# Kernel optimization log

Hardware: AMD Instinct MI355X
Metric: run time of the kernel (lower is better)

The kernel has to match this reference:

```python
import jax, jax.numpy as jnp
import numpy as np

H, I, B = 256, 128, 512

def setup_inputs() -> dict:
    key = jax.random.key(0)
    ks = jax.random.split(key, 24)
    n = lambda k, shp, s=1.0: jax.random.normal(k, shp, dtype=jnp.float32) * s
    inp = {
        "x": n(ks[0], (B, I)),
        "hx": n(ks[1], (B, H), 0.1),
        "cx": n(ks[2], (B, H, H), 0.1),
        # input->gate weights (hidden, input), xavier-like scale
        "Wii": n(ks[3], (H, I), (2.0 / (H + I)) ** 0.5),
        "Wif": n(ks[4], (H, I), (2.0 / (H + I)) ** 0.5),
        "Wig": n(ks[5], (H, I), (2.0 / (H + I)) ** 0.5),
        "Wio": n(ks[6], (H, I), (2.0 / (H + I)) ** 0.5),
        # hidden->gate weights (hidden, hidden), ~orthogonal scale
        "Whi": n(ks[7], (H, H), H ** -0.5),
        "Whit": n(ks[8], (H, H), H ** -0.5),
        "Whf": n(ks[9], (H, H), H ** -0.5),
        "Whft": n(ks[10], (H, H), H ** -0.5),
        "Whc": n(ks[11], (H, H), H ** -0.5),
        "Whct": n(ks[12], (H, H), H ** -0.5),
        "Who": n(ks[13], (H, H), H ** -0.5),
        "Uinv": n(ks[14], (H, H), H ** -0.5),
        "Vtinv": n(ks[15], (H, H), H ** -0.5),
        # biases: bi/bf/bg are full (H,H) matrices, bo is (H,1)
        "bi": jnp.zeros((H, H), jnp.float32),
        "bf": jnp.zeros((H, H), jnp.float32),
        "bg": jnp.zeros((H, H), jnp.float32),
        "bo": jnp.zeros((H, 1), jnp.float32),
    }
    return inp


def reference(x, hx, cx, Wii, Wif, Wig, Wio, Whi, Whit, Whf, Whft, Whc, Whct, Who, Uinv, Vtinv, bi, bf, bg, bo):
    # W @ diag(v) @ M^T  ==  einsum('hi,bi,gi->bhg', W, v, M)
    def sandwich(Wx, Wh, Wht, b):
        # (Wx*x) @ Wx^T + (Wh*hx) @ Wht^T + b  -> (B,H,H)
        xt = jnp.einsum('hi,bi,gi->bhg', Wx, x, Wx)
        ht = jnp.einsum('hj,bj,gj->bhg', Wh, hx, Wht)
        return xt + ht + b

    i = jax.nn.sigmoid(sandwich(Wii, Whi, Whit, bi))
    f = jax.nn.sigmoid(sandwich(Wif, Whf, Whft, bf))
    g = jnp.tanh(sandwich(Wig, Whc, Whct, bg))
    # o: ordinary vector gate (B,H)
    o = jax.nn.sigmoid(jnp.einsum('hi,bi->bh', Wio, x)
                       + jnp.einsum('hj,bj->bh', Who, hx) + bo[:, 0])
    cx_new = f * cx + i * g                     # (B,H,H)
    # diag(Uinv @ cx_new @ Vtinv) per batch element -> (B,H)
    proj_down = jnp.einsum('ij,bjk,ki->bi', Uinv, cx_new, Vtinv)
    hx_new = o * jax.nn.sigmoid(proj_down)
    return hx_new
```

## Files before the change

kernel.cpp:

```cpp
#include <hip/hip_runtime.h>
#include <hip/hip_bf16.h>

#define Hh 256
#define Ii 128
#define KF 384
#define LDSB 72

typedef __attribute__((ext_vector_type(8))) short bf16x8;
typedef __attribute__((ext_vector_type(4))) float f32x4;
typedef unsigned short u16;
typedef unsigned int u32;

__device__ inline u16 f2bf(float f) {
  u32 u = __float_as_uint(f);
  u += 0x7FFFu + ((u >> 16) & 1u);
  return (u16)(u >> 16);
}
__device__ inline u32 pack_bf16x2(float a, float b) {
  __hip_bfloat162 h = __float22bfloat162_rn(make_float2(a, b));
  u32 r; __builtin_memcpy(&r, &h, 4); return r;
}
__device__ inline u32 scale2(u32 packed, float va, float vb) {
  float lo = __uint_as_float(packed << 16) * va;
  float hi = __uint_as_float(packed & 0xFFFF0000u) * vb;
  return pack_bf16x2(lo, hi);
}
__device__ inline float sigm(float x) { return 1.0f / (1.0f + __expf(-x)); }
__device__ inline float tanh_f(float x) { return 1.0f - 2.0f / (1.0f + __expf(2.0f * x)); }

union U32x4 { bf16x8 f; u32 d[4]; uint4 v; };

__global__ __launch_bounds__(256) void k_prep(
    const float* __restrict__ Wii, const float* __restrict__ Wif, const float* __restrict__ Wig,
    const float* __restrict__ Whi, const float* __restrict__ Whit,
    const float* __restrict__ Whf, const float* __restrict__ Whft,
    const float* __restrict__ Whc, const float* __restrict__ Whct,
    const float* __restrict__ Vtinv, const float* __restrict__ Uinv,
    u16* __restrict__ RW, u16* __restrict__ CW, u16* __restrict__ Vtt,
    float* __restrict__ UinvP, float* __restrict__ proj) {
  const int tid = threadIdx.x, bx = blockIdx.x, y = blockIdx.y;
  if (y < 3) {
    const float* WX  = (y == 0) ? Wii : (y == 1 ? Wif : Wig);
    const float* WHr = (y == 0) ? Whi : (y == 1 ? Whf : Whc);
    const float* WHt = (y == 0) ? Whit : (y == 1 ? Whft : Whct);
    u16* rw = RW + y * Hh * KF;
    u16* cw = CW + y * Hh * KF;
#pragma unroll
    for (int it = 0; it < 4; ++it) {
      int idx = it * 24576 + bx * 256 + tid;
      int h = idx / KF, t = idx - h * KF;
      float a, c;
      if (t < Ii) { a = WX[h * Ii + t]; c = a; }
      else        { a = WHr[h * Hh + t - Ii]; c = WHt[h * Hh + t - Ii]; }
      rw[idx] = f2bf(a);
      cw[idx] = f2bf(c);
    }
  } else if (y == 3) {
    if (bx < 64) {
      __shared__ u16 tbuf[32][33];
      const int c = tid & 31, r8 = tid >> 5;
      const int tr = bx >> 3, tc = bx & 7;
#pragma unroll
      for (int rr = r8; rr < 32; rr += 8)
        tbuf[rr][c] = f2bf(Vtinv[(tc * 32 + rr) * Hh + tr * 32 + c]);
      __syncthreads();
#pragma unroll
      for (int rr = r8; rr < 32; rr += 8)
        Vtt[(tr * 32 + rr) * Hh + tc * 32 + c] = tbuf[c][rr];
    } else if (bx < 96) {
      const int base = (bx - 64) * 256 + tid;
      const float4 z = {0.f, 0.f, 0.f, 0.f};
#pragma unroll
      for (int it = 0; it < 4; ++it)
        *(float4*)(proj + (size_t)(it * 8192 + base) * 4) = z;
    }
  } else {
    if (bx < 32) {
      const int base = (bx * 256 + tid) * 8;
#pragma unroll
      for (int e8 = 0; e8 < 8; ++e8) {
        int f = base + e8;
        int t512 = f >> 7;
        int e = f & 127;
        int ti = e >> 5;
        int rem = e & 31;
        int tjl = rem >> 2;
        int rr = rem & 3;
        int wv = t512 >> 6;
        int ln = t512 & 63;
        int qd = ln >> 4;
        int r15v = ln & 15;
        int i = (wv & 3) * 64 + ti * 16 + qd * 4 + rr;
        int j = (wv >> 2) * 128 + tjl * 16 + r15v;
        UinvP[f] = Uinv[i * Hh + j];
      }
    }
  }
}

__global__ __launch_bounds__(512) void k_main(
    const float* __restrict__ x, const float* __restrict__ hx, const float* __restrict__ cx,
    const u16* __restrict__ RW, const u16* __restrict__ CW, const u16* __restrict__ Vtt,
    const float* __restrict__ bi, const float* __restrict__ bfm, const float* __restrict__ bg,
    const float* __restrict__ UinvP, float* __restrict__ proj) {
  __shared__ u16 sB[2 * 64 * LDSB];
  __shared__ u16 sP[256 * LDSB];
  __shared__ float sV[KF];
  __shared__ float sPart[8][64];

  const int tid  = threadIdx.x;
  const int b    = blockIdx.x >> 2;
  const int kb   = blockIdx.x & 3;
  const int k0   = kb * 64;
  const int lane = tid & 63;
  const int w    = tid >> 6;
  const int r15  = lane & 15;
  const int quad = lane >> 4;
  const int brow = tid >> 3, bcg = tid & 7;

  if (tid < Ii) sV[tid] = x[b * Ii + tid];
  if (tid < Hh) sV[Ii + tid] = hx[b * Hh + tid];

  const u16* rwp[3] = {RW + 2 * Hh * KF, RW, RW + 1 * Hh * KF};
  const u16* cwp[3] = {CW + 2 * Hh * KF, CW, CW + 1 * Hh * KF};
  const float* bp3[3] = {bg, bi, bfm};
  const float* cx_b = cx + (size_t)b * Hh * Hh;

  U32x4 m;
  m.v = *(const uint4*)(cwp[0] + (size_t)(k0 + brow) * KF + bcg * 8);
  __syncthreads();
  {
    U32x4 o;
    const float4 va = *(const float4*)(&sV[bcg * 8]);
    const float4 vb = *(const float4*)(&sV[bcg * 8 + 4]);
    o.d[0] = scale2(m.d[0], va.x, va.y); o.d[1] = scale2(m.d[1], va.z, va.w);
    o.d[2] = scale2(m.d[2], vb.x, vb.y); o.d[3] = scale2(m.d[3], vb.z, vb.w);
    *(uint4*)(&sB[brow * LDSB + bcg * 8]) = o.v;
  }
  __syncthreads();

  float p[2][4][4];
  const size_t wrow = (size_t)(w * 32 + r15) * KF;

#pragma unroll
  for (int ph = 0; ph < 3; ++ph) {
    f32x4 acc[2][4];
#pragma unroll
    for (int ja = 0; ja < 2; ++ja)
#pragma unroll
      for (int tk = 0; tk < 4; ++tk)
#pragma unroll
        for (int r = 0; r < 4; ++r) acc[ja][tk][r] = 0.0f;

#pragma unroll
    for (int kc = 0; kc < 6; ++kc) {
      const int sc  = ph * 6 + kc;
      const int cur = sc & 1;
      const int t0  = kc * 64;
      const int nph = (kc < 5) ? ph : (ph < 2 ? ph + 1 : 0);
      const int nt0 = (kc < 5) ? t0 + 64 : 0;
      U32x4 mn;
      if (sc < 17)
        mn.v = *(const uint4*)(cwp[nph] + (size_t)(k0 + brow) * KF + nt0 + bcg * 8);
      bf16x8 wf[2][2];
#pragma unroll
      for (int ja = 0; ja < 2; ++ja)
#pragma unroll
        for (int ks = 0; ks < 2; ++ks)
          wf[ja][ks] = *(const bf16x8*)(rwp[ph] + wrow + (size_t)ja * 16 * KF + t0 + ks * 32 + quad * 8);
#pragma unroll
      for (int ks = 0; ks < 2; ++ks) {
        bf16x8 sf[4];
#pragma unroll
        for (int tk = 0; tk < 4; ++tk)
          sf[tk] = *(const bf16x8*)(&sB[cur * (64 * LDSB) + (tk * 16 + r15) * LDSB + ks * 32 + quad * 8]);
#pragma unroll
        for (int tk = 0; tk < 4; ++tk) {
          acc[0][tk] = __builtin_amdgcn_mfma_f32_16x16x32_bf16(sf[tk], wf[0][ks], acc[0][tk], 0, 0, 0);
          acc[1][tk] = __builtin_amdgcn_mfma_f32_16x16x32_bf16(sf[tk], wf[1][ks], acc[1][tk], 0, 0, 0);
        }
      }
      if (sc < 17) {
        U32x4 o;
        const float4 va = *(const float4*)(&sV[nt0 + bcg * 8]);
        const float4 vb = *(const float4*)(&sV[nt0 + bcg * 8 + 4]);
        o.d[0] = scale2(mn.d[0], va.x, va.y); o.d[1] = scale2(mn.d[1], va.z, va.w);
        o.d[2] = scale2(mn.d[2], vb.x, vb.y); o.d[3] = scale2(mn.d[3], vb.z, vb.w);
        *(uint4*)(&sB[(cur ^ 1) * (64 * LDSB) + brow * LDSB + bcg * 8]) = o.v;
      }
      if (kc == 5) {
        const float* bp = bp3[ph];
#pragma unroll
        for (int ja = 0; ja < 2; ++ja) {
          const int jg = w * 32 + ja * 16 + r15;
          const float* bpr = bp + (size_t)jg * Hh + k0 + quad * 4;
          const float* cxr = cx_b + (size_t)jg * Hh + k0 + quad * 4;
#pragma unroll
          for (int tk = 0; tk < 4; ++tk) {
            const float4 bv = *(const float4*)(bpr + tk * 16);
            if (ph == 0) {
#pragma unroll
              for (int r = 0; r < 4; ++r)
                p[ja][tk][r] = tanh_f(acc[ja][tk][r] + ((const float*)&bv)[r]);
            } else if (ph == 1) {
#pragma unroll
              for (int r = 0; r < 4; ++r)
                p[ja][tk][r] *= sigm(acc[ja][tk][r] + ((const float*)&bv)[r]);
            } else {
              const float4 cv = *(const float4*)(cxr + tk * 16);
              float cc[4];
#pragma unroll
              for (int r = 0; r < 4; ++r)
                cc[r] = sigm(acc[ja][tk][r] + ((const float*)&bv)[r]) * ((const float*)&cv)[r] + p[ja][tk][r];
              uint2 pk;
              pk.x = pack_bf16x2(cc[0], cc[1]);
              pk.y = pack_bf16x2(cc[2], cc[3]);
              *(uint2*)(&sP[jg * LDSB + tk * 16 + quad * 4]) = pk;
            }
          }
        }
      }
      __syncthreads();
    }
  }

  const int islab = (w & 3) * 64;
  const int jhb   = (w >> 2) * 128;
  const float* up = UinvP + (size_t)tid * 128;
  float racc[4][4];
#pragma unroll
  for (int ti = 0; ti < 4; ++ti)
#pragma unroll
    for (int r = 0; r < 4; ++r) racc[ti][r] = 0.0f;

#pragma unroll
  for (int tjg = 0; tjg < 2; ++tjg) {
    bf16x8 fbp[2][4];
#pragma unroll
    for (int ks = 0; ks < 2; ++ks)
#pragma unroll
      for (int tjj = 0; tjj < 4; ++tjj)
        fbp[ks][tjj] = *(const bf16x8*)(&sP[(jhb + (tjg * 4 + tjj) * 16 + r15) * LDSB + ks * 32 + quad * 8]);
#pragma unroll
    for (int ti = 0; ti < 4; ++ti) {
      const u16* vrow = Vtt + (size_t)(islab + ti * 16 + r15) * Hh + k0 + quad * 8;
      const bf16x8 va0 = *(const bf16x8*)vrow;
      const bf16x8 va1 = *(const bf16x8*)(vrow + 32);
      f32x4 pacc[4];
#pragma unroll
      for (int tjj = 0; tjj < 4; ++tjj)
#pragma unroll
        for (int r = 0; r < 4; ++r) pacc[tjj][r] = 0.0f;
#pragma unroll
      for (int tjj = 0; tjj < 4; ++tjj)
        pacc[tjj] = __builtin_amdgcn_mfma_f32_16x16x32_bf16(va0, fbp[0][tjj], pacc[tjj], 0, 0, 0);
#pragma unroll
      for (int tjj = 0; tjj < 4; ++tjj)
        pacc[tjj] = __builtin_amdgcn_mfma_f32_16x16x32_bf16(va1, fbp[1][tjj], pacc[tjj], 0, 0, 0);
#pragma unroll
      for (int tjj = 0; tjj < 4; ++tjj) {
        const float4 uu = *(const float4*)(up + ti * 32 + (tjg * 4 + tjj) * 4);
#pragma unroll
        for (int r = 0; r < 4; ++r)
          racc[ti][r] += pacc[tjj][r] * ((const float*)&uu)[r];
      }
    }
  }

#pragma unroll
  for (int ti = 0; ti < 4; ++ti)
#pragma unroll
    for (int r = 0; r < 4; ++r) {
      float v = racc[ti][r];
      v += __shfl_xor(v, 1);
      v += __shfl_xor(v, 2);
      v += __shfl_xor(v, 4);
      v += __shfl_xor(v, 8);
      if (r15 == 0) sPart[w][ti * 16 + quad * 4 + r] = v;
    }
  __syncthreads();
  if (tid < Hh)
    atomicAdd(&proj[b * Hh + tid], sPart[tid >> 6][tid & 63] + sPart[(tid >> 6) + 4][tid & 63]);
}

__global__ __launch_bounds__(256) void k_out(
    const float* __restrict__ x, const float* __restrict__ hx,
    const float* __restrict__ Wio, const float* __restrict__ Who,
    const float* __restrict__ bo, const float* __restrict__ proj,
    float* __restrict__ out) {
  __shared__ float sv[KF];
  const int b = blockIdx.x, tid = threadIdx.x;
  const int lane = tid & 63, w = tid >> 6;
  if (tid < Ii) sv[tid] = x[b * Ii + tid];
  sv[Ii + tid] = hx[b * Hh + tid];
  __syncthreads();
  for (int rr = 0; rr < 64; ++rr) {
    const int h = w * 64 + rr;
    float p = Wio[h * Ii + lane]        * sv[lane]
            + Wio[h * Ii + 64 + lane]   * sv[64 + lane]
            + Who[h * Hh + lane]        * sv[128 + lane]
            + Who[h * Hh + 64 + lane]   * sv[192 + lane]
            + Who[h * Hh + 128 + lane]  * sv[256 + lane]
            + Who[h * Hh + 192 + lane]  * sv[320 + lane];
    p += __shfl_xor(p, 32);
    p += __shfl_xor(p, 16);
    p += __shfl_xor(p, 8);
    p += __shfl_xor(p, 4);
    p += __shfl_xor(p, 2);
    p += __shfl_xor(p, 1);
    if (lane == 0)
      out[b * Hh + h] = sigm(p + bo[h]) * sigm(proj[b * Hh + h]);
  }
}

extern "C" void kernel_launch(void* const* d_in, const int* in_sizes, int n_in,
                              void* d_out, int out_size, void* d_ws, size_t ws_size,
                              hipStream_t stream) {
  (void)in_sizes; (void)n_in; (void)out_size; (void)ws_size;
  const float* x    = (const float*)d_in[0];
  const float* hx   = (const float*)d_in[1];
  const float* cx   = (const float*)d_in[2];
  const float* Wii  = (const float*)d_in[3];
  const float* Wif  = (const float*)d_in[4];
  const float* Wig  = (const float*)d_in[5];
  const float* Wio  = (const float*)d_in[6];
  const float* Whi  = (const float*)d_in[7];
  const float* Whit = (const float*)d_in[8];
  const float* Whf  = (const float*)d_in[9];
  const float* Whft = (const float*)d_in[10];
  const float* Whc  = (const float*)d_in[11];
  const float* Whct = (const float*)d_in[12];
  const float* Who  = (const float*)d_in[13];
  const float* Uinv = (const float*)d_in[14];
  const float* Vtinv= (const float*)d_in[15];
  const float* bi   = (const float*)d_in[16];
  const float* bf   = (const float*)d_in[17];
  const float* bg   = (const float*)d_in[18];
  const float* bo   = (const float*)d_in[19];
  float* out = (float*)d_out;

  u16* RW    = (u16*)d_ws;
  u16* CW    = RW + 3 * Hh * KF;
  u16* Vtt   = CW + 3 * Hh * KF;
  float* UinvP = (float*)(Vtt + Hh * Hh);
  float* proj  = UinvP + Hh * Hh;

  k_prep<<<dim3(96, 5), 256, 0, stream>>>(Wii, Wif, Wig, Whi, Whit, Whf, Whft, Whc, Whct,
                                          Vtinv, Uinv, RW, CW, Vtt, UinvP, proj);
  k_main<<<2048, 512, 0, stream>>>(x, hx, cx, RW, CW, Vtt, bi, bf, bg, UinvP, proj);
  k_out<<<512, 256, 0, stream>>>(x, hx, Wio, Who, bo, proj, out);
}
```

Baseline: 583.4 us.

## Retile gate GEMM with wider K chunks and 4x2 warp tiles, union LDS buffers

The gate-stage GEMM now uses K chunks of 192 instead of 64, so each phase takes 2 steps instead of 6, cutting the number of __syncthreads and double-buffer refills. Warps are rearranged into a 4x2 (j by k) grid with 4x2 MFMA tiles, so each B fragment loaded from LDS is reused across four weight fragments. The B staging buffer and the P buffer share one LDS union, and the final f-gate/cell update moves after the loop with an extra barrier. In exchange, register pressure rises (more global loads per step, larger staging buffers), and the padded stride of 200 may cause LDS bank conflicts.

Result: slower. 708.9 us (+21.5%).

```diff
diff --git a/kernel.cpp b/kernel.cpp
--- a/kernel.cpp
+++ b/kernel.cpp
@@ -5,6 +5,8 @@
 #define Ii 128
 #define KF 384
 #define LDSB 72
+#define BK 192
+#define SBST 200
 
 typedef __attribute__((ext_vector_type(8))) short bf16x8;
 typedef __attribute__((ext_vector_type(4))) float f32x4;
@@ -27,8 +29,6 @@
 }
 __device__ inline float sigm(float x) { return 1.0f / (1.0f + __expf(-x)); }
 __device__ inline float tanh_f(float x) { return 1.0f - 2.0f / (1.0f + __expf(2.0f * x)); }
-
-union U32x4 { bf16x8 f; u32 d[4]; uint4 v; };
 
 __global__ __launch_bounds__(256) void k_prep(
     const float* __restrict__ Wii, const float* __restrict__ Wif, const float* __restrict__ Wig,
@@ -103,8 +103,10 @@
     const u16* __restrict__ RW, const u16* __restrict__ CW, const u16* __restrict__ Vtt,
     const float* __restrict__ bi, const float* __restrict__ bfm, const float* __restrict__ bg,
     const float* __restrict__ UinvP, float* __restrict__ proj) {
-  __shared__ u16 sB[2 * 64 * LDSB];
-  __shared__ u16 sP[256 * LDSB];
+  __shared__ union {
+    u16 B[2][64][SBST];
+    u16 P[256][LDSB];
+  } sU;
   __shared__ float sV[KF];
   __shared__ float sPart[8][64];
 
@@ -114,9 +116,12 @@
   const int k0   = kb * 64;
   const int lane = tid & 63;
   const int w    = tid >> 6;
+  const int wj   = w >> 1;
+  const int wk   = w & 1;
   const int r15  = lane & 15;
   const int quad = lane >> 4;
-  const int brow = tid >> 3, bcg = tid & 7;
+  const int srow = tid >> 3;
+  const int scg  = tid & 7;
 
   if (tid < Ii) sV[tid] = x[b * Ii + tid];
   if (tid < Hh) sV[Ii + tid] = hx[b * Hh + tid];
@@ -126,96 +131,122 @@
   const float* bp3[3] = {bg, bi, bfm};
   const float* cx_b = cx + (size_t)b * Hh * Hh;
 
-  U32x4 m;
-  m.v = *(const uint4*)(cwp[0] + (size_t)(k0 + brow) * KF + bcg * 8);
+  uint4 m0, m1, m2;
+  {
+    const u16* src = cwp[0] + (size_t)(k0 + srow) * KF + scg * 24;
+    m0 = *(const uint4*)src;
+    m1 = *(const uint4*)(src + 8);
+    m2 = *(const uint4*)(src + 16);
+  }
   __syncthreads();
   {
-    U32x4 o;
-    const float4 va = *(const float4*)(&sV[bcg * 8]);
-    const float4 vb = *(const float4*)(&sV[bcg * 8 + 4]);
-    o.d[0] = scale2(m.d[0], va.x, va.y); o.d[1] = scale2(m.d[1], va.z, va.w);
-    o.d[2] = scale2(m.d[2], vb.x, vb.y); o.d[3] = scale2(m.d[3], vb.z, vb.w);
-    *(uint4*)(&sB[brow * LDSB + bcg * 8]) = o.v;
+    const float* vp = &sV[scg * 24];
+    const float4 v0 = *(const float4*)(vp);
+    const float4 v1 = *(const float4*)(vp + 4);
+    const float4 v2 = *(const float4*)(vp + 8);
+    const float4 v3 = *(const float4*)(vp + 12);
+    const float4 v4 = *(const float4*)(vp + 16);
+    const float4 v5 = *(const float4*)(vp + 20);
+    uint4 o0, o1, o2;
+    o0.x = scale2(m0.x, v0.x, v0.y); o0.y = scale2(m0.y, v0.z, v0.w);
+    o0.z = scale2(m0.z, v1.x, v1.y); o0.w = scale2(m0.w, v1.z, v1.w);
+    o1.x = scale2(m1.x, v2.x, v2.y); o1.y = scale2(m1.y, v2.z, v2.w);
+    o1.z = scale2(m1.z, v3.x, v3.y); o1.w = scale2(m1.w, v3.z, v3.w);
+    o2.x = scale2(m2.x, v4.x, v4.y); o2.y = scale2(m2.y, v4.z, v4.w);
+    o2.z = scale2(m2.z, v5.x, v5.y); o2.w = scale2(m2.w, v5.z, v5.w);
+    u16* dst = &sU.B[0][srow][scg * 24];
+    *(uint4*)dst = o0;
+    *(uint4*)(dst + 8) = o1;
+    *(uint4*)(dst + 16) = o2;
   }
   __syncthreads();
 
-  float p[2][4][4];
-  const size_t wrow = (size_t)(w * 32 + r15) * KF;
+  float p[4][2][4];
+  f32x4 acc[4][2];
+  const size_t jrow = (size_t)(wj * 64 + r15) * KF;
+  const int ar = wk * 32 + r15;
 
 #pragma unroll
   for (int ph = 0; ph < 3; ++ph) {
-    f32x4 acc[2][4];
-#pragma unroll
-    for (int ja = 0; ja < 2; ++ja)
-#pragma unroll
-      for (int tk = 0; tk < 4; ++tk)
+#pragma unroll
+    for (int ja = 0; ja < 4; ++ja)
+#pragma unroll
+      for (int tk = 0; tk < 2; ++tk)
 #pragma unroll
         for (int r = 0; r < 4; ++r) acc[ja][tk][r] = 0.0f;
 
 #pragma unroll
-    for (int kc = 0; kc < 6; ++kc) {
-      const int sc  = ph * 6 + kc;
+    for (int kc = 0; kc < 2; ++kc) {
+      const int sc  = ph * 2 + kc;
       const int cur = sc & 1;
-      const int t0  = kc * 64;
-      const int nph = (kc < 5) ? ph : (ph < 2 ? ph + 1 : 0);
-      const int nt0 = (kc < 5) ? t0 + 64 : 0;
-      U32x4 mn;
-      if (sc < 17)
-        mn.v = *(const uint4*)(cwp[nph] + (size_t)(k0 + brow) * KF + nt0 + bcg * 8);
-      bf16x8 wf[2][2];
-#pragma unroll
-      for (int ja = 0; ja < 2; ++ja)
-#pragma unroll
-        for (int ks = 0; ks < 2; ++ks)
-          wf[ja][ks] = *(const bf16x8*)(rwp[ph] + wrow + (size_t)ja * 16 * KF + t0 + ks * 32 + quad * 8);
-#pragma unroll
-      for (int ks = 0; ks < 2; ++ks) {
-        bf16x8 sf[4];
-#pragma unroll
-        for (int tk = 0; tk < 4; ++tk)
-          sf[tk] = *(const bf16x8*)(&sB[cur * (64 * LDSB) + (tk * 16 + r15) * LDSB + ks * 32 + quad * 8]);
-#pragma unroll
-        for (int tk = 0; tk < 4; ++tk) {
-          acc[0][tk] = __builtin_amdgcn_mfma_f32_16x16x32_bf16(sf[tk], wf[0][ks], acc[0][tk], 0, 0, 0);
-          acc[1][tk] = __builtin_amdgcn_mfma_f32_16x16x32_bf16(sf[tk], wf[1][ks], acc[1][tk], 0, 0, 0);
-        }
-      }
-      if (sc < 17) {
-        U32x4 o;
-        const float4 va = *(const float4*)(&sV[nt0 + bcg * 8]);
-        const float4 vb = *(const float4*)(&sV[nt0 + bcg * 8 + 4]);
-        o.d[0] = scale2(mn.d[0], va.x, va.y); o.d[1] = scale2(mn.d[1], va.z, va.w);
-        o.d[2] = scale2(mn.d[2], vb.x, vb.y); o.d[3] = scale2(mn.d[3], vb.z, vb.w);
-        *(uint4*)(&sB[(cur ^ 1) * (64 * LDSB) + brow * LDSB + bcg * 8]) = o.v;
-      }
-      if (kc == 5) {
+      const int t0  = kc * BK;
+      uint4 n0, n1, n2;
+      if (sc < 5) {
+        const int nsc = sc + 1;
+        const int nph = nsc >> 1;
+        const int nt0 = (nsc & 1) * BK;
+        const u16* src = cwp[nph] + (size_t)(k0 + srow) * KF + nt0 + scg * 24;
+        n0 = *(const uint4*)src;
+        n1 = *(const uint4*)(src + 8);
+        n2 = *(const uint4*)(src + 16);
+      }
+      const u16* rb = rwp[ph] + jrow + t0 + quad * 8;
+#pragma unroll
+      for (int ksl = 0; ksl < 6; ++ksl) {
+        const bf16x8 sf0 = *(const bf16x8*)(&sU.B[cur][ar][ksl * 32 + quad * 8]);
+        const bf16x8 sf1 = *(const bf16x8*)(&sU.B[cur][ar + 16][ksl * 32 + quad * 8]);
+        const bf16x8 wf0 = *(const bf16x8*)(rb + ksl * 32);
+        const bf16x8 wf1 = *(const bf16x8*)(rb + 16 * KF + ksl * 32);
+        const bf16x8 wf2 = *(const bf16x8*)(rb + 32 * KF + ksl * 32);
+        const bf16x8 wf3 = *(const bf16x8*)(rb + 48 * KF + ksl * 32);
+        acc[0][0] = __builtin_amdgcn_mfma_f32_16x16x32_bf16(sf0, wf0, acc[0][0], 0, 0, 0);
+        acc[0][1] = __builtin_amdgcn_mfma_f32_16x16x32_bf16(sf1, wf0, acc[0][1], 0, 0, 0);
+        acc[1][0] = __builtin_amdgcn_mfma_f32_16x16x32_bf16(sf0, wf1, acc[1][0], 0, 0, 0);
+        acc[1][1] = __builtin_amdgcn_mfma_f32_16x16x32_bf16(sf1, wf1, acc[1][1], 0, 0, 0);
+        acc[2][0] = __builtin_amdgcn_mfma_f32_16x16x32_bf16(sf0, wf2, acc[2][0], 0, 0, 0);
+        acc[2][1] = __builtin_amdgcn_mfma_f32_16x16x32_bf16(sf1, wf2, acc[2][1], 0, 0, 0);
+        acc[3][0] = __builtin_amdgcn_mfma_f32_16x16x32_bf16(sf0, wf3, acc[3][0], 0, 0, 0);
+        acc[3][1] = __builtin_amdgcn_mfma_f32_16x16x32_bf16(sf1, wf3, acc[3][1], 0, 0, 0);
+      }
+      if (sc < 5) {
+        const int nsc = sc + 1;
+        const int nt0 = (nsc & 1) * BK;
+        const float* vp = &sV[nt0 + scg * 24];
+        const float4 v0 = *(const float4*)(vp);
+        const float4 v1 = *(const float4*)(vp + 4);
+        const float4 v2 = *(const float4*)(vp + 8);
+        const float4 v3 = *(const float4*)(vp + 12);
+        const float4 v4 = *(const float4*)(vp + 16);
+        const float4 v5 = *(const float4*)(vp + 20);
+        uint4 o0, o1, o2;
+        o0.x = scale2(n0.x, v0.x, v0.y); o0.y = scale2(n0.y, v0.z, v0.w);
+        o0.z = scale2(n0.z, v1.x, v1.y); o0.w = scale2(n0.w, v1.z, v1.w);
+        o1.x = scale2(n1.x, v2.x, v2.y); o1.y = scale2(n1.y, v2.z, v2.w);
+        o1.z = scale2(n1.z, v3.x, v3.y); o1.w = scale2(n1.w, v3.z, v3.w);
+        o2.x = scale2(n2.x, v4.x, v4.y); o2.y = scale2(n2.y, v4.z, v4.w);
+        o2.z = scale2(n2.z, v5.x, v5.y); o2.w = scale2(n2.w, v5.z, v5.w);
+        u16* dst = &sU.B[cur ^ 1][srow][scg * 24];
+        *(uint4*)dst = o0;
+        *(uint4*)(dst + 8) = o1;
+        *(uint4*)(dst + 16) = o2;
+      }
+      if (ph < 2 && kc == 1) {
         const float* bp = bp3[ph];
 #pragma unroll
-        for (int ja = 0; ja < 2; ++ja) {
-          const int jg = w * 32 + ja * 16 + r15;
-          const float* bpr = bp + (size_t)jg * Hh + k0 + quad * 4;
-          const float* cxr = cx_b + (size_t)jg * Hh + k0 + quad * 4;
-#pragma unroll
-          for (int tk = 0; tk < 4; ++tk) {
+        for (int ja = 0; ja < 4; ++ja) {
+          const int jg = wj * 64 + ja * 16 + r15;
+          const float* bpr = bp + (size_t)jg * Hh + k0 + wk * 32 + quad * 4;
+#pragma unroll
+          for (int tk = 0; tk < 2; ++tk) {
             const float4 bv = *(const float4*)(bpr + tk * 16);
             if (ph == 0) {
 #pragma unroll
               for (int r = 0; r < 4; ++r)
                 p[ja][tk][r] = tanh_f(acc[ja][tk][r] + ((const float*)&bv)[r]);
-            } else if (ph == 1) {
+            } else {
 #pragma unroll
               for (int r = 0; r < 4; ++r)
                 p[ja][tk][r] *= sigm(acc[ja][tk][r] + ((const float*)&bv)[r]);
-            } else {
-              const float4 cv = *(const float4*)(cxr + tk * 16);
-              float cc[4];
-#pragma unroll
-              for (int r = 0; r < 4; ++r)
-                cc[r] = sigm(acc[ja][tk][r] + ((const float*)&bv)[r]) * ((const float*)&cv)[r] + p[ja][tk][r];
-              uint2 pk;
-              pk.x = pack_bf16x2(cc[0], cc[1]);
-              pk.y = pack_bf16x2(cc[2], cc[3]);
-              *(uint2*)(&sP[jg * LDSB + tk * 16 + quad * 4]) = pk;
             }
           }
         }
@@ -223,6 +254,27 @@
       __syncthreads();
     }
   }
+
+#pragma unroll
+  for (int ja = 0; ja < 4; ++ja) {
+    const int jg = wj * 64 + ja * 16 + r15;
+    const float* bpr = bfm + (size_t)jg * Hh + k0 + wk * 32 + quad * 4;
+    const float* cxr = cx_b + (size_t)jg * Hh + k0 + wk * 32 + quad * 4;
+#pragma unroll
+    for (int tk = 0; tk < 2; ++tk) {
+      const float4 bv = *(const float4*)(bpr + tk * 16);
+      const float4 cv = *(const float4*)(cxr + tk * 16);
+      float cc[4];
+#pragma unroll
+      for (int r = 0; r < 4; ++r)
+        cc[r] = sigm(acc[ja][tk][r] + ((const float*)&bv)[r]) * ((const float*)&cv)[r] + p[ja][tk][r];
+      uint2 pk;
+      pk.x = pack_bf16x2(cc[0], cc[1]);
+      pk.y = pack_bf16x2(cc[2], cc[3]);
+      *(uint2*)(&sU.P[jg][wk * 32 + tk * 16 + quad * 4]) = pk;
+    }
+  }
+  __syncthreads();
 
   const int islab = (w & 3) * 64;
   const int jhb   = (w >> 2) * 128;
@@ -240,7 +292,7 @@
     for (int ks = 0; ks < 2; ++ks)
 #pragma unroll
       for (int tjj = 0; tjj < 4; ++tjj)
-        fbp[ks][tjj] = *(const bf16x8*)(&sP[(jhb + (tjg * 4 + tjj) * 16 + r15) * LDSB + ks * 32 + quad * 8]);
+        fbp[ks][tjj] = *(const bf16x8*)(&sU.P[jhb + (tjg * 4 + tjj) * 16 + r15][ks * 32 + quad * 8]);
 #pragma unroll
     for (int ti = 0; ti < 4; ++ti) {
       const u16* vrow = Vtt + (size_t)(islab + ti * 16 + r15) * Hh + k0 + quad * 8;
```

## Tile pre-packed bf16 weights into 64-wide blocks and alias LDS buffers

Applied to the files above, without the earlier changes.

The prep kernel now writes the row-side and column-side bf16 weight matrices in 64-column tiled layouts. Each k_main chunk load therefore becomes one contiguous block instead of strided rows of length 384. The sB staging buffer and the sP cx_new buffer now share one LDS union, which cuts shared-memory use and may allow more blocks per CU. The final f-gate/cx epilogue moves out of the phase loop to after the last barrier, so it can safely overwrite the aliased buffer, at the cost of one extra __syncthreads.

Result: no change. 578.6 us (-0.8%).

```diff
diff --git a/kernel.cpp b/kernel.cpp
--- a/kernel.cpp
+++ b/kernel.cpp
@@ -52,8 +52,8 @@
       float a, c;
       if (t < Ii) { a = WX[h * Ii + t]; c = a; }
       else        { a = WHr[h * Hh + t - Ii]; c = WHt[h * Hh + t - Ii]; }
-      rw[idx] = f2bf(a);
-      cw[idx] = f2bf(c);
+      rw[(t >> 6) * 16384 + h * 64 + (t & 63)] = f2bf(a);
+      cw[(h >> 6) * 24576 + (t >> 6) * 4096 + (h & 63) * 64 + (t & 63)] = f2bf(c);
     }
   } else if (y == 3) {
     if (bx < 64) {
@@ -103,8 +103,10 @@
     const u16* __restrict__ RW, const u16* __restrict__ CW, const u16* __restrict__ Vtt,
     const float* __restrict__ bi, const float* __restrict__ bfm, const float* __restrict__ bg,
     const float* __restrict__ UinvP, float* __restrict__ proj) {
-  __shared__ u16 sB[2 * 64 * LDSB];
-  __shared__ u16 sP[256 * LDSB];
+  __shared__ union {
+    u16 B[2][64][LDSB];
+    u16 P[256][LDSB];
+  } sU;
   __shared__ float sV[KF];
   __shared__ float sPart[8][64];
 
@@ -116,35 +118,35 @@
   const int w    = tid >> 6;
   const int r15  = lane & 15;
   const int quad = lane >> 4;
-  const int brow = tid >> 3, bcg = tid & 7;
 
   if (tid < Ii) sV[tid] = x[b * Ii + tid];
   if (tid < Hh) sV[Ii + tid] = hx[b * Hh + tid];
 
   const u16* rwp[3] = {RW + 2 * Hh * KF, RW, RW + 1 * Hh * KF};
-  const u16* cwp[3] = {CW + 2 * Hh * KF, CW, CW + 1 * Hh * KF};
-  const float* bp3[3] = {bg, bi, bfm};
+  const u16* cwp[3] = {CW + 2 * Hh * KF + kb * 24576, CW + kb * 24576,
+                       CW + 1 * Hh * KF + kb * 24576};
+  const float* bp3[2] = {bg, bi};
   const float* cx_b = cx + (size_t)b * Hh * Hh;
 
   U32x4 m;
-  m.v = *(const uint4*)(cwp[0] + (size_t)(k0 + brow) * KF + bcg * 8);
+  m.v = *(const uint4*)(cwp[0] + tid * 8);
   __syncthreads();
   {
     U32x4 o;
-    const float4 va = *(const float4*)(&sV[bcg * 8]);
-    const float4 vb = *(const float4*)(&sV[bcg * 8 + 4]);
+    const float4 va = *(const float4*)(&sV[(tid & 7) * 8]);
+    const float4 vb = *(const float4*)(&sV[(tid & 7) * 8 + 4]);
     o.d[0] = scale2(m.d[0], va.x, va.y); o.d[1] = scale2(m.d[1], va.z, va.w);
     o.d[2] = scale2(m.d[2], vb.x, vb.y); o.d[3] = scale2(m.d[3], vb.z, vb.w);
-    *(uint4*)(&sB[brow * LDSB + bcg * 8]) = o.v;
+    *(uint4*)(&sU.B[0][tid >> 3][(tid & 7) * 8]) = o.v;
   }
   __syncthreads();
 
   float p[2][4][4];
-  const size_t wrow = (size_t)(w * 32 + r15) * KF;
+  f32x4 acc[2][4];
+  const int wfoff = (w * 32 + r15) * 64 + quad * 8;
 
 #pragma unroll
   for (int ph = 0; ph < 3; ++ph) {
-    f32x4 acc[2][4];
 #pragma unroll
     for (int ja = 0; ja < 2; ++ja)
 #pragma unroll
@@ -156,24 +158,26 @@
     for (int kc = 0; kc < 6; ++kc) {
       const int sc  = ph * 6 + kc;
       const int cur = sc & 1;
-      const int t0  = kc * 64;
       const int nph = (kc < 5) ? ph : (ph < 2 ? ph + 1 : 0);
-      const int nt0 = (kc < 5) ? t0 + 64 : 0;
+      const int nkc = (kc < 5) ? kc + 1 : 0;
       U32x4 mn;
       if (sc < 17)
-        mn.v = *(const uint4*)(cwp[nph] + (size_t)(k0 + brow) * KF + nt0 + bcg * 8);
+        mn.v = *(const uint4*)(cwp[nph] + nkc * 4096 + tid * 8);
       bf16x8 wf[2][2];
-#pragma unroll
-      for (int ja = 0; ja < 2; ++ja)
-#pragma unroll
-        for (int ks = 0; ks < 2; ++ks)
-          wf[ja][ks] = *(const bf16x8*)(rwp[ph] + wrow + (size_t)ja * 16 * KF + t0 + ks * 32 + quad * 8);
+      {
+        const u16* rb = rwp[ph] + kc * 16384 + wfoff;
+#pragma unroll
+        for (int ja = 0; ja < 2; ++ja)
+#pragma unroll
+          for (int ks = 0; ks < 2; ++ks)
+            wf[ja][ks] = *(const bf16x8*)(rb + ja * 1024 + ks * 32);
+      }
 #pragma unroll
       for (int ks = 0; ks < 2; ++ks) {
         bf16x8 sf[4];
 #pragma unroll
         for (int tk = 0; tk < 4; ++tk)
-          sf[tk] = *(const bf16x8*)(&sB[cur * (64 * LDSB) + (tk * 16 + r15) * LDSB + ks * 32 + quad * 8]);
+          sf[tk] = *(const bf16x8*)(&sU.B[cur][tk * 16 + r15][ks * 32 + quad * 8]);
 #pragma unroll
         for (int tk = 0; tk < 4; ++tk) {
           acc[0][tk] = __builtin_amdgcn_mfma_f32_16x16x32_bf16(sf[tk], wf[0][ks], acc[0][tk], 0, 0, 0);
@@ -182,19 +186,19 @@
       }
       if (sc < 17) {
         U32x4 o;
-        const float4 va = *(const float4*)(&sV[nt0 + bcg * 8]);
-        const float4 vb = *(const float4*)(&sV[nt0 + bcg * 8 + 4]);
+        const int nt0 = nkc * 64;
+        const float4 va = *(const float4*)(&sV[nt0 + (tid & 7) * 8]);
+        const float4 vb = *(const float4*)(&sV[nt0 + (tid & 7) * 8 + 4]);
         o.d[0] = scale2(mn.d[0], va.x, va.y); o.d[1] = scale2(mn.d[1], va.z, va.w);
         o.d[2] = scale2(mn.d[2], vb.x, vb.y); o.d[3] = scale2(mn.d[3], vb.z, vb.w);
-        *(uint4*)(&sB[(cur ^ 1) * (64 * LDSB) + brow * LDSB + bcg * 8]) = o.v;
-      }
-      if (kc == 5) {
+        *(uint4*)(&sU.B[cur ^ 1][tid >> 3][(tid & 7) * 8]) = o.v;
+      }
+      if (ph < 2 && kc == 5) {
         const float* bp = bp3[ph];
 #pragma unroll
         for (int ja = 0; ja < 2; ++ja) {
           const int jg = w * 32 + ja * 16 + r15;
           const float* bpr = bp + (size_t)jg * Hh + k0 + quad * 4;
-          const float* cxr = cx_b + (size_t)jg * Hh + k0 + quad * 4;
 #pragma unroll
           for (int tk = 0; tk < 4; ++tk) {
             const float4 bv = *(const float4*)(bpr + tk * 16);
@@ -202,20 +206,10 @@
 #pragma unroll
               for (int r = 0; r < 4; ++r)
                 p[ja][tk][r] = tanh_f(acc[ja][tk][r] + ((const float*)&bv)[r]);
-            } else if (ph == 1) {
+            } else {
 #pragma unroll
               for (int r = 0; r < 4; ++r)
                 p[ja][tk][r] *= sigm(acc[ja][tk][r] + ((const float*)&bv)[r]);
-            } else {
-              const float4 cv = *(const float4*)(cxr + tk * 16);
-              float cc[4];
-#pragma unroll
-              for (int r = 0; r < 4; ++r)
-                cc[r] = sigm(acc[ja][tk][r] + ((const float*)&bv)[r]) * ((const float*)&cv)[r] + p[ja][tk][r];
-              uint2 pk;
-              pk.x = pack_bf16x2(cc[0], cc[1]);
-              pk.y = pack_bf16x2(cc[2], cc[3]);
-              *(uint2*)(&sP[jg * LDSB + tk * 16 + quad * 4]) = pk;
             }
           }
         }
@@ -223,6 +217,27 @@
       __syncthreads();
     }
   }
+
+#pragma unroll
+  for (int ja = 0; ja < 2; ++ja) {
+    const int jg = w * 32 + ja * 16 + r15;
+    const float* bpr = bfm + (size_t)jg * Hh + k0 + quad * 4;
+    const float* cxr = cx_b + (size_t)jg * Hh + k0 + quad * 4;
+#pragma unroll
+    for (int tk = 0; tk < 4; ++tk) {
+      const float4 bv = *(const float4*)(bpr + tk * 16);
+      const float4 cv = *(const float4*)(cxr + tk * 16);
+      float cc[4];
+#pragma unroll
+      for (int r = 0; r < 4; ++r)
+        cc[r] = sigm(acc[ja][tk][r] + ((const float*)&bv)[r]) * ((const float*)&cv)[r] + p[ja][tk][r];
+      uint2 pk;
+      pk.x = pack_bf16x2(cc[0], cc[1]);
+      pk.y = pack_bf16x2(cc[2], cc[3]);
+      *(uint2*)(&sU.P[jg][tk * 16 + quad * 4]) = pk;
+    }
+  }
+  __syncthreads();
 
   const int islab = (w & 3) * 64;
   const int jhb   = (w >> 2) * 128;
@@ -240,7 +255,7 @@
     for (int ks = 0; ks < 2; ++ks)
 #pragma unroll
       for (int tjj = 0; tjj < 4; ++tjj)
-        fbp[ks][tjj] = *(const bf16x8*)(&sP[(jhb + (tjg * 4 + tjj) * 16 + r15) * LDSB + ks * 32 + quad * 8]);
+        fbp[ks][tjj] = *(const bf16x8*)(&sU.P[jhb + (tjg * 4 + tjj) * 16 + r15][ks * 32 + quad * 8]);
 #pragma unroll
     for (int ti = 0; ti < 4; ++ti) {
       const u16* vrow = Vtt + (size_t)(islab + ti * 16 + r15) * Hh + k0 + quad * 8;
```
